# Kernel tuning notes

Hardware: AMD Instinct MI355X
Metric: run time of the kernel (lower is better)

Reference implementation:

```python
import jax, jax.numpy as jnp
import numpy as np

KERNEL = 9
EPS = 1e-5


def build_time_adj(t, kernel=KERNEL):
    # Faithful port of time_edge_index + utils.add_self_loops (all weights 1).
    # At[target, source] = 1 ; PyG edge list rows were [source=i, target=neighbor].
    p = (kernel - 1) // 2
    edges = []
    for i in range(t):
        if i < p:
            num_zeros_before = p - i
            elems = kernel - 1 - num_zeros_before
            before = i
            after = elems - before
            for j in range(before, 0, -1):
                edges.append((i, i - j))
            for j in range(after, 0, -1):
                edges.append((i, i + j))
        elif t - i <= p:
            num_zeros_after = p - (t - i) + 1
            elems = kernel - 1 - num_zeros_after
            before = kernel - 1 - p
            after = elems - before
            for j in range(before, 0, -1):
                edges.append((i, i - j))
            for j in range(after, 0, -1):
                edges.append((i, i + j))
        else:
            for j in range(1, p + 1):
                edges.append((i, i - j))
                edges.append((i, i + j))
    At = np.zeros((t, t), dtype=np.float32)
    for s, tg in edges:
        At[tg, s] = 1.0
    At[np.arange(t), np.arange(t)] = 1.0  # add_self_loops
    return At


def setup_inputs() -> dict:
    key = jax.random.key(0)
    ks = jax.random.split(key, 8)
    B, T, V, C = 64, 300, 25, 64
    x = jax.random.normal(ks[0], (B, T, V, C), dtype=jnp.float32)
    A = jax.random.uniform(ks[1], (3, V, V), dtype=jnp.float32)
    edge_importance = jnp.ones((3, V, V), dtype=jnp.float32)
    scale = 0.125  # ~xavier for 64x64
    W1 = jax.random.normal(ks[2], (C, C), dtype=jnp.float32) * scale
    W2 = jax.random.normal(ks[3], (C, C), dtype=jnp.float32) * scale
    W3 = jax.random.normal(ks[4], (C, C), dtype=jnp.float32) * scale
    Wt = jax.random.normal(ks[5], (C, C), dtype=jnp.float32) * scale
    b1 = jnp.zeros((C,), jnp.float32)
    b2 = jnp.zeros((C,), jnp.float32)
    b3 = jnp.zeros((C,), jnp.float32)
    bt = jnp.zeros((C,), jnp.float32)
    gamma = jnp.ones((C,), jnp.float32)
    beta = jnp.zeros((C,), jnp.float32)
    return {"x": x, "A": A, "edge_importance": edge_importance,
            "W1": W1, "b1": b1, "W2": W2, "b2": b2, "W3": W3, "b3": b3,
            "Wt": Wt, "bt": bt, "gamma": gamma, "beta": beta}


def reference(x, A, edge_importance, W1, b1, W2, b2, W3, b3, Wt, bt, gamma, beta):
    B, T, V, C = x.shape
    I = jnp.eye(V, dtype=x.dtype)
    Ae = A * edge_importance  # [3,V,V]

    # ---- Net_nodes: 3 spatial GCNConv branches summed (gcn_norm, self-loops) ----
    out = jnp.zeros((B, T, V, W1.shape[1]), dtype=x.dtype)
    for Ai, W, b in ((Ae[0], W1, b1), (Ae[1], W2, b2), (Ae[2], W3, b3)):
        Ad = Ai * (1.0 - I) + I                      # fill_diag(adj, 1.0)
        d = Ad.sum(axis=1)
        dinv = jnp.where(d > 0, d ** -0.5, 0.0)
        An = dinv[:, None] * Ad * dinv[None, :]      # D^-1/2 (A+I) D^-1/2
        out = out + jnp.einsum('vu,btuc->btvc', An, x @ W) + b

    def bn(h):  # BatchNorm2d over (B,T,V) per channel, training-mode stats
        m = h.mean(axis=(0, 1, 2))
        v = h.var(axis=(0, 1, 2))
        return (h - m) * jax.lax.rsqrt(v + EPS) * gamma + beta

    h = jax.nn.relu(bn(out))

    # ---- temporal GCNConv (normalize=False, unit edge weights, self loops) ----
    At = jnp.asarray(build_time_adj(T))              # [T,T] banded 0/1
    h = jnp.einsum('ts,bsvc->btvc', At, h @ Wt) + bt

    h = bn(h)  # same bn_2d module reused; dropout is identity in eval
    # residual=False, stride=1 -> x_res = 0, no sampling
    return jax.nn.relu(h)
```

## Files before the change

kernel.cpp:

```cpp
#include <hip/hip_runtime.h>

typedef unsigned short u16;
typedef unsigned int   u32;
typedef _Float16       f16;
typedef _Float16 f16x8 __attribute__((ext_vector_type(8)));
typedef float    f32x4 __attribute__((ext_vector_type(4)));

#define B_  64
#define T_  300
#define V_  25
#define C_  64
#define ROWS (B_*T_)
#define ROWE (V_*C_)
#define NSTAT 480000.0f
#define EPS_ 1e-5f
#define TTILE 30
#define K2BLK 1200
#define NWID  4800

__device__ __forceinline__ float b2f(u16 u) {
    union { u32 i; float f; } v; v.i = ((u32)u) << 16; return v.f;
}
__device__ __forceinline__ u16 f2b(float f) {
    union { float f; u32 i; } v; v.f = f;
    u32 x = v.i;
    u32 r = x + 0x7fffu + ((x >> 16) & 1u);
    return (u16)(r >> 16);
}
__device__ __forceinline__ u32 pk2h(float a, float b) {
    union { f16 h[2]; u32 u; } p;
    p.h[0] = (f16)a; p.h[1] = (f16)b;
    return p.u;
}
__device__ __forceinline__ u16 h2u(float v) {
    union { f16 h; u16 u; } p; p.h = (f16)v; return p.u;
}
__device__ __forceinline__ float u2h(u16 u) {
    union { u16 u; f16 h; } p; p.u = u; return (float)p.h;
}

template<bool F32>
__device__ __forceinline__ float ldv(const void* p, size_t i) {
    if (F32) return ((const float*)p)[i];
    return b2f(((const u16*)p)[i]);
}

template<bool F32> struct Geo { static const int STR = F32 ? 3200 : 1600; };

__global__ void k0_detect(const void* W1raw, int* flag)
{
    __shared__ float red[256];
    const u16* p = (const u16*)W1raw;
    float mx = 0.0f;
    for (int i = threadIdx.x; i < 4096; i += 256) {
        float v = fabsf(b2f(p[i]));
        if (v == v) mx = fmaxf(mx, v);
    }
    red[threadIdx.x] = mx;
    __syncthreads();
    for (int s = 128; s > 0; s >>= 1) {
        if (threadIdx.x < s) red[threadIdx.x] = fmaxf(red[threadIdx.x], red[threadIdx.x + s]);
        __syncthreads();
    }
    if (threadIdx.x == 0) flag[0] = (red[0] > 1e10f) ? 1 : 0;
}

template<bool F32>
__global__ void k1_prep(const int* __restrict__ flag,
                        const void* A, const void* E,
                        const void* W1, const void* W2, const void* W3,
                        const void* Wt,
                        const void* b1, const void* b2, const void* b3,
                        u16* __restrict__ anf, u16* __restrict__ wcatT,
                        u16* __restrict__ wtT, float* __restrict__ bsum)
{
    if (flag[0] != (F32 ? 1 : 0)) return;
    __shared__ float dinvL[75];
    const int tid = threadIdx.x;
    if (tid < 75) {
        int i = tid / 25, v = tid % 25;
        float d = 1.0f;
        for (int u = 0; u < 25; ++u)
            if (u != v) d += ldv<F32>(A, (i*25+v)*25+u) * ldv<F32>(E, (i*25+v)*25+u);
        dinvL[tid] = (d > 0.0f) ? rsqrtf(d) : 0.0f;
    }
    __syncthreads();
    for (int idx = tid; idx < 3072; idx += 256) {
        int fr = idx >> 9, lane = (idx >> 3) & 63, j = idx & 7;
        int i = fr >> 1, nt = fr & 1;
        int v = nt*16 + (lane & 15);
        int u = ((lane >> 4) << 3) + j;
        float val = 0.0f;
        if (v < 25 && u < 25) {
            float ad = (u == v) ? 1.0f
                     : ldv<F32>(A, (i*25+v)*25+u) * ldv<F32>(E, (i*25+v)*25+u);
            val = dinvL[i*25+v] * ad * dinvL[i*25+u];
        }
        anf[idx] = h2u(val);
    }
    for (int idx = tid; idx < 13824; idx += 256) {
        int i = idx / 4608;
        int rem = idx - i*4608;
        int c = rem / 72, k = rem - (rem/72)*72;
        float val = 0.0f;
        if (k < 64) {
            const void* W = (i == 0) ? W1 : ((i == 1) ? W2 : W3);
            val = ldv<F32>(W, k*64 + c);
        }
        wcatT[idx] = h2u(val);
    }
    for (int idx = tid; idx < 4608; idx += 256) {
        int c = idx / 72, k = idx - (idx/72)*72;
        float val = (k < 64) ? ldv<F32>(Wt, k*64 + c) : 0.0f;
        wtT[idx] = h2u(val);
    }
    if (tid < 64) bsum[tid] = ldv<F32>(b1, tid) + ldv<F32>(b2, tid) + ldv<F32>(b3, tid);
}

template<bool F32>
__global__ __launch_bounds__(256, 3) void k2_mfma(
    const int* __restrict__ flag, const void* x,
    const u16* __restrict__ wcatT, const u16* __restrict__ anf,
    u16* __restrict__ out1, u16* __restrict__ halo, float* __restrict__ p1)
{
    if (flag[0] != (F32 ? 1 : 0)) return;
    const int STR = Geo<F32>::STR;

    __shared__ f16 xfS[4][32*64];
    __shared__ u16 xwS[4][64*64];

    const int tid = threadIdx.x, lane = tid & 63, w = tid >> 6;
    const int lo = lane & 15, hi = lane >> 4;
    f16* xf = xfS[w];
    u16* xw = xwS[w];

    for (int q = lane; q < 224; q += 64) ((u32*)xf)[800 + q] = 0u;

    const int wid = blockIdx.x*4 + w;

    float ss[16], sq[16];
    #pragma unroll
    for (int i = 0; i < 16; ++i) { ss[i] = 0.0f; sq[i] = 0.0f; }

    #pragma unroll 1
    for (int rr = 0; rr < 4; ++rr) {
        const int row = wid*4 + rr;

        for (int q = lane; q < 200; q += 64) {
            const int u = q >> 3, g = q & 7;
            float v0,v1,v2,v3,v4,v5,v6,v7;
            if (F32) {
                float4 a4 = ((const float4*)x)[(size_t)row*400 + q*2];
                float4 b4 = ((const float4*)x)[(size_t)row*400 + q*2 + 1];
                v0=a4.x; v1=a4.y; v2=a4.z; v3=a4.w;
                v4=b4.x; v5=b4.y; v6=b4.z; v7=b4.w;
            } else {
                union { uint4 u4; u16 s[8]; } t4;
                t4.u4 = ((const uint4*)x)[(size_t)row*200 + q];
                v0=b2f(t4.s[0]); v1=b2f(t4.s[1]); v2=b2f(t4.s[2]); v3=b2f(t4.s[3]);
                v4=b2f(t4.s[4]); v5=b2f(t4.s[5]); v6=b2f(t4.s[6]); v7=b2f(t4.s[7]);
            }
            uint4 st = make_uint4(pk2h(v0,v1), pk2h(v2,v3), pk2h(v4,v5), pk2h(v6,v7));
            *(uint4*)&xf[u*64 + ((g ^ (u & 7)) << 3)] = st;
        }

        f32x4 acc[4][2];
        #pragma unroll
        for (int m = 0; m < 4; ++m) {
            acc[m][0] = f32x4{0.f,0.f,0.f,0.f};
            acc[m][1] = f32x4{0.f,0.f,0.f,0.f};
        }

        #pragma unroll 1
        for (int i = 0; i < 3; ++i) {
            f16x8 wfr[4][2];
            #pragma unroll
            for (int nt = 0; nt < 4; ++nt)
                #pragma unroll
                for (int ks = 0; ks < 2; ++ks)
                    wfr[nt][ks] = *(const f16x8*)&wcatT[
                        (size_t)(i*64 + nt*16 + lo)*72 + ks*32 + (hi << 3)];
            f16x8 an0 = *(const f16x8*)&anf[((i*2 + 0)*64 + lane)*8];
            f16x8 an1 = *(const f16x8*)&anf[((i*2 + 1)*64 + lane)*8];

            #pragma unroll
            for (int mt = 0; mt < 2; ++mt) {
                const int mrow = mt*16 + lo;
                f16x8 a0 = *(const f16x8*)&xf[mrow*64 + ((hi ^ (lo & 7)) << 3)];
                f16x8 a1 = *(const f16x8*)&xf[mrow*64 + (((4|hi) ^ (lo & 7)) << 3)];
                const int gu  = mt*2 + (hi >> 1);
                const int off = (hi & 1)*4;
                #pragma unroll
                for (int nt = 0; nt < 4; ++nt) {
                    f32x4 d = f32x4{0.f,0.f,0.f,0.f};
                    d = __builtin_amdgcn_mfma_f32_16x16x32_f16(a0, wfr[nt][0], d, 0, 0, 0);
                    d = __builtin_amdgcn_mfma_f32_16x16x32_f16(a1, wfr[nt][1], d, 0, 0, 0);
                    const int c = nt*16 + lo;
                    *(uint2*)&xw[c*64 + ((gu ^ (lo & 7)) << 3) + off] =
                        make_uint2(pk2h(d[0], d[1]), pk2h(d[2], d[3]));
                }
            }

            #pragma unroll
            for (int mt2 = 0; mt2 < 4; ++mt2) {
                f16x8 a = *(const f16x8*)&xw[(mt2*16 + lo)*64 + ((hi ^ (lo & 7)) << 3)];
                acc[mt2][0] = __builtin_amdgcn_mfma_f32_16x16x32_f16(a, an0, acc[mt2][0], 0, 0, 0);
                acc[mt2][1] = __builtin_amdgcn_mfma_f32_16x16x32_f16(a, an1, acc[mt2][1], 0, 0, 0);
            }
        }

        const int b = row / T_;
        const int t = row - b*T_;
        const int tm = t % TTILE;
        const bool hbd = (tm < 4) || (tm >= TTILE - 4);
        u16* hrow = nullptr;
        if (hbd) {
            const int slot = tm < 4 ? tm : tm - 22;
            hrow = halo + (((size_t)b*10 + t/TTILE)*8 + slot)*ROWE;
        }
        u16* orow = out1 + (size_t)row*STR;
        #pragma unroll
        for (int mt2 = 0; mt2 < 4; ++mt2) {
            const int c0 = mt2*16 + hi*4;
            #pragma unroll
            for (int nt2 = 0; nt2 < 2; ++nt2) {
                const int v = nt2*16 + lo;
                const float o0 = acc[mt2][nt2][0];
                const float o1 = acc[mt2][nt2][1];
                const float o2 = acc[mt2][nt2][2];
                const float o3 = acc[mt2][nt2][3];
                ss[mt2*4+0] += o0; sq[mt2*4+0] += o0*o0;
                ss[mt2*4+1] += o1; sq[mt2*4+1] += o1*o1;
                ss[mt2*4+2] += o2; sq[mt2*4+2] += o2*o2;
                ss[mt2*4+3] += o3; sq[mt2*4+3] += o3*o3;
                if (v < 25) {
                    ushort4 pk;
                    pk.x = f2b(o0); pk.y = f2b(o1); pk.z = f2b(o2); pk.w = f2b(o3);
                    *(ushort4*)&orow[v*64 + c0] = pk;
                    if (hbd) *(ushort4*)&hrow[v*64 + c0] = pk;
                }
            }
        }
    }

    #pragma unroll
    for (int si = 0; si < 16; ++si) {
        #pragma unroll
        for (int off = 1; off < 16; off <<= 1) {
            ss[si] += __shfl_xor(ss[si], off);
            sq[si] += __shfl_xor(sq[si], off);
        }
    }
    if (lo == 0) {
        #pragma unroll
        for (int si = 0; si < 16; ++si) {
            const int c = (si >> 2)*16 + hi*4 + (si & 3);
            p1[(size_t)wid*128 + c]      = ss[si];
            p1[(size_t)wid*128 + 64 + c] = sq[si];
        }
    }
}

__global__ __launch_bounds__(128) void k_reduce(const float* __restrict__ in,
                                                int n, float* __restrict__ outq)
{
    const int t = threadIdx.x;
    float s = 0.0f;
    for (int r = blockIdx.x; r < n; r += 64) s += in[(size_t)r*128 + t];
    outq[(size_t)blockIdx.x*128 + t] = s;
}

template<bool F32>
__global__ void k_bnstats(const int* __restrict__ flag,
                          const float* __restrict__ q,
                          const void* gamma, const void* beta,
                          const float* __restrict__ mb, int useb,
                          float* __restrict__ scale, float* __restrict__ shift)
{
    if (flag[0] != (F32 ? 1 : 0)) return;
    __shared__ float redL[512];
    const int tid = threadIdx.x, c = tid & 63, g = tid >> 6;
    float s = 0.0f, ssq = 0.0f;
    for (int r = g; r < 64; r += 4) { s += q[r*128 + c]; ssq += q[r*128 + 64 + c]; }
    redL[g*64 + c] = s; redL[256 + g*64 + c] = ssq;
    __syncthreads();
    if (tid < 64) {
        const float S  = redL[tid] + redL[64+tid] + redL[128+tid] + redL[192+tid];
        const float SS = redL[256+tid] + redL[320+tid] + redL[384+tid] + redL[448+tid];
        const float my  = S / NSTAT;
        const float var = SS / NSTAT - my*my;
        const float m   = my + (useb ? mb[tid] : 0.0f);
        const float rstd = rsqrtf(var + EPS_);
        const float sc = ldv<F32>(gamma, tid) * rstd;
        scale[tid] = sc;
        shift[tid] = ldv<F32>(beta, tid) - m * sc;
    }
}

template<bool F32>
__device__ __forceinline__ const u16* row_ptr(const u16* out1, const u16* halo,
                                              int b, int s, int t0)
{
    if (s >= t0 && s < t0 + TTILE)
        return &out1[((size_t)b*T_ + s) * Geo<F32>::STR];
    const int tile = s / TTILE, rem = s % TTILE;
    const int slot = rem < 4 ? rem : rem - 22;
    return &halo[(((size_t)b*10 + tile)*8 + slot) * ROWE];
}

template<bool F32>
__global__ __launch_bounds__(256, 3) void k3_temporal(
    const int* __restrict__ flag,
    u16* out1, const u16* __restrict__ halo,
    const u16* __restrict__ wtT, const void* bt,
    const float* __restrict__ sc1, const float* __restrict__ sh1,
    float* __restrict__ p2)
{
    if (flag[0] != (F32 ? 1 : 0)) return;
    const int STR = Geo<F32>::STR;

    __shared__ u16   ring[10*1600];
    __shared__ f16   hsumH[32*72];
    __shared__ u16   zL[1600];
    __shared__ float redL[256];

    const int tid = threadIdx.x, lane = tid & 63, w = tid >> 6;
    const int b = blockIdx.y, t0 = blockIdx.x * TTILE;
    const bool act = (tid < 200);

    for (int i = tid; i < 252; i += 256) ((u32*)&hsumH[25*72])[i] = 0u;

    float hacc[8];
    #pragma unroll
    for (int e = 0; e < 8; ++e) hacc[e] = 0.0f;
    const int c0u = (tid*8) & 63;
    const int vrow = tid >> 3;
    float S1[8], H1[8];
    #pragma unroll
    for (int e = 0; e < 8; ++e) { S1[e] = sc1[c0u+e]; H1[e] = sh1[c0u+e]; }

    const int ntp = w >> 1, mt = w & 1;
    f16x8 wfr[2][2];
    #pragma unroll
    for (int ntl = 0; ntl < 2; ++ntl)
        #pragma unroll
        for (int ks = 0; ks < 2; ++ks)
            wfr[ntl][ks] = *(const f16x8*)&wtT[
                ((ntp*2+ntl)*16 + (lane & 15))*72 + ks*32 + ((lane >> 4) << 3)];
    float btv[2];
    #pragma unroll
    for (int ntl = 0; ntl < 2; ++ntl)
        btv[ntl] = ldv<F32>(bt, (ntp*2+ntl)*16 + (lane & 15));

    {
        int slo = t0 - 4; if (slo < 0) slo = 0;
        for (int s = slo; s <= t0 + 4; ++s) {
            const u16* xr = row_ptr<F32>(out1, halo, b, s, t0);
            if (act) {
                uint4 xv = *(const uint4*)&xr[tid*8];
                const u16* xs = (const u16*)&xv;
                u16 hb[8];
                #pragma unroll
                for (int e = 0; e < 8; ++e) {
                    float hv = fmaf(b2f(xs[e]), S1[e], H1[e]);
                    hv = hv > 0.0f ? hv : 0.0f;
                    hb[e] = f2b(hv);
                    hacc[e] += b2f(hb[e]);
                }
                *(uint4*)&ring[(s%10)*1600 + tid*8] = *(uint4*)hb;
            }
        }
        if (act) {
            u16 hs[8];
            #pragma unroll
            for (int e = 0; e < 8; ++e) hs[e] = h2u(hacc[e]);
            *(uint4*)&hsumH[vrow*72 + c0u] = *(uint4*)hs;
        }
    }
    __syncthreads();

    float zs[2] = {0.f, 0.f}, zq[2] = {0.f, 0.f};

    for (int t = t0; t < t0 + TTILE; ++t) {
        {
            const int arow = (mt*16 + (lane & 15))*72 + ((lane >> 4) << 3);
            f16x8 a0 = *(const f16x8*)&hsumH[arow];
            f16x8 a1 = *(const f16x8*)&hsumH[arow + 32];
            #pragma unroll
            for (int ntl = 0; ntl < 2; ++ntl) {
                f32x4 d = f32x4{btv[ntl], btv[ntl], btv[ntl], btv[ntl]};
                d = __builtin_amdgcn_mfma_f32_16x16x32_f16(a0, wfr[ntl][0], d, 0, 0, 0);
                d = __builtin_amdgcn_mfma_f32_16x16x32_f16(a1, wfr[ntl][1], d, 0, 0, 0);
                const int cc = (ntp*2+ntl)*16 + (lane & 15);
                #pragma unroll
                for (int j = 0; j < 4; ++j) {
                    const int v = mt*16 + ((lane >> 4) << 2) + j;
                    if (v < 25) {
                        zs[ntl] += d[j]; zq[ntl] += d[j]*d[j];
                        zL[v*64 + cc] = h2u(d[j]);
                    }
                }
            }
        }
        __syncthreads();

        if (tid < 200)
            *(uint4*)&out1[((size_t)b*T_ + t)*STR + tid*8] = ((const uint4*)zL)[tid];

        if (t + 1 < t0 + TTILE) {
            const int snew = t + 5, sold = t - 4;
            if (act) {
                if (snew < T_) {
                    const u16* xr = row_ptr<F32>(out1, halo, b, snew, t0);
                    uint4 xv = *(const uint4*)&xr[tid*8];
                    const u16* xs = (const u16*)&xv;
                    u16 hb[8];
                    #pragma unroll
                    for (int e = 0; e < 8; ++e) {
                        float hv = fmaf(b2f(xs[e]), S1[e], H1[e]);
                        hv = hv > 0.0f ? hv : 0.0f;
                        hb[e] = f2b(hv);
                        hacc[e] += b2f(hb[e]);
                    }
                    *(uint4*)&ring[(snew%10)*1600 + tid*8] = *(uint4*)hb;
                }
                if (sold >= 0) {
                    uint4 ov = *(const uint4*)&ring[(sold%10)*1600 + tid*8];
                    const u16* os = (const u16*)&ov;
                    #pragma unroll
                    for (int e = 0; e < 8; ++e) hacc[e] -= b2f(os[e]);
                }
                u16 hs[8];
                #pragma unroll
                for (int e = 0; e < 8; ++e) hs[e] = h2u(hacc[e]);
                *(uint4*)&hsumH[vrow*72 + c0u] = *(uint4*)hs;
            }
        }
        __syncthreads();
    }

    #pragma unroll
    for (int ntl = 0; ntl < 2; ++ntl) {
        #pragma unroll
        for (int off = 16; off < 64; off <<= 1) {
            zs[ntl] += __shfl_xor(zs[ntl], off);
            zq[ntl] += __shfl_xor(zq[ntl], off);
        }
    }
    if (lane < 16) {
        redL[w*32 + lane]            = zs[0];
        redL[w*32 + 16 + lane]       = zs[1];
        redL[128 + w*32 + lane]      = zq[0];
        redL[128 + w*32 + 16 + lane] = zq[1];
    }
    __syncthreads();
    if (tid < 64) {
        const int c = tid;
        const int ntg = c >> 4, pr = ntg >> 1, ntl = ntg & 1, l = c & 15;
        const int w0 = pr*2, w1 = pr*2 + 1;
        float s = redL[w0*32 + ntl*16 + l] + redL[w1*32 + ntl*16 + l];
        float q = redL[128 + w0*32 + ntl*16 + l] + redL[128 + w1*32 + ntl*16 + l];
        const int blk = blockIdx.y * (T_/TTILE) + blockIdx.x;
        p2[(size_t)blk*128 + c]      = s;
        p2[(size_t)blk*128 + 64 + c] = q;
    }
}

template<bool F32>
__global__ __launch_bounds__(256) void k4_final(
    const int* __restrict__ flag,
    const float* __restrict__ sc2, const float* __restrict__ sh2,
    void* outp)
{
    if (flag[0] != (F32 ? 1 : 0)) return;
    const int tid = threadIdx.x;

    if (!F32) {
        const size_t NQ = (size_t)ROWS * 200;
        const size_t stride = (size_t)gridDim.x * blockDim.x;
        size_t q = (size_t)blockIdx.x * blockDim.x + tid;
        const int c0 = ((int)(q & 7)) * 8;
        float S2[8], H2[8];
        #pragma unroll
        for (int e = 0; e < 8; ++e) { S2[e] = sc2[c0+e]; H2[e] = sh2[c0+e]; }
        u16* z = (u16*)outp;
        for (; q < NQ; q += stride) {
            union { uint4 u4; u16 s[8]; } zv;
            zv.u4 = *(const uint4*)&z[q*8];
            u16 ob[8];
            #pragma unroll
            for (int e = 0; e < 8; ++e) {
                float oo = fmaf(u2h(zv.s[e]), S2[e], H2[e]);
                ob[e] = f2b(oo > 0.0f ? oo : 0.0f);
            }
            *(uint4*)&z[q*8] = *(uint4*)ob;
        }
    } else {
        const int STR = Geo<true>::STR;
        const int c0u = (tid*8) & 63;
        float S2[8], H2[8];
        #pragma unroll
        for (int e = 0; e < 8; ++e) { S2[e] = sc2[c0u+e]; H2[e] = sh2[c0u+e]; }
        const int r0 = blockIdx.x * 10;
        u16* z = (u16*)outp;
        for (int r = 0; r < 10; ++r) {
            const int row = r0 + r;
            uint4 zv;
            if (tid < 200) zv = *(const uint4*)&z[(size_t)row*STR + tid*8];
            __syncthreads();
            if (tid < 200) {
                const u16* zp = (const u16*)&zv;
                float o[8];
                #pragma unroll
                for (int e = 0; e < 8; ++e) {
                    float oo = fmaf(u2h(zp[e]), S2[e], H2[e]);
                    o[e] = oo > 0.0f ? oo : 0.0f;
                }
                float* dst = (float*)outp + (size_t)row*ROWE + tid*8;
                *(float4*)dst     = float4{o[0], o[1], o[2], o[3]};
                *(float4*)(dst+4) = float4{o[4], o[5], o[6], o[7]};
            }
            __syncthreads();
        }
    }
}

extern "C" void kernel_launch(void* const* d_in, const int* in_sizes, int n_in,
                              void* d_out, int out_size, void* d_ws, size_t ws_size,
                              hipStream_t stream)
{
    const void* x     = d_in[0];
    const void* A     = d_in[1];
    const void* E     = d_in[2];
    const void* W1    = d_in[3];
    const void* b1    = d_in[4];
    const void* W2    = d_in[5];
    const void* b2    = d_in[6];
    const void* W3    = d_in[7];
    const void* b3    = d_in[8];
    const void* Wt    = d_in[9];
    const void* bt    = d_in[10];
    const void* gamma = d_in[11];
    const void* beta  = d_in[12];

    u16* out1 = (u16*)d_out;

    int*   flag = (int*)d_ws;
    float* wsf  = (float*)d_ws;
    float* bsum = wsf + 4;
    float* sc1  = bsum + 64;
    float* sh1  = sc1 + 64;
    float* sc2  = sh1 + 64;
    float* sh2  = sc2 + 64;
    float* p1   = sh2 + 64;
    float* p2   = p1 + (size_t)NWID*128;
    float* q1   = p2 + 640*128;
    float* q2   = q1 + 64*128;
    u16*  halo  = (u16*)(q2 + 64*128);
    u16*  wcatT = halo + (size_t)5120*1600;
    u16*  anf   = wcatT + 13824;
    u16*  wtT   = anf + 3072;

    const long NX = (long)B_*T_*V_*C_;
    int mode = -1;
    if (n_in > 0) {
        if      (in_sizes[0] == (int)(NX*2)) mode = 0;
        else if (in_sizes[0] == (int)(NX*4)) mode = 1;
    }
    const bool do_b = (mode != 1), do_f = (mode != 0);

    hipLaunchKernelGGL(k0_detect, dim3(1), dim3(256), 0, stream, W1, flag);

    if (do_b) hipLaunchKernelGGL(k1_prep<false>, dim3(1), dim3(256), 0, stream,
                       flag, A, E, W1, W2, W3, Wt, b1, b2, b3, anf, wcatT, wtT, bsum);
    if (do_f) hipLaunchKernelGGL(k1_prep<true>, dim3(1), dim3(256), 0, stream,
                       flag, A, E, W1, W2, W3, Wt, b1, b2, b3, anf, wcatT, wtT, bsum);

    if (do_b) hipLaunchKernelGGL(k2_mfma<false>, dim3(K2BLK), dim3(256), 0, stream,
                       flag, x, wcatT, anf, out1, halo, p1);
    if (do_f) hipLaunchKernelGGL(k2_mfma<true>, dim3(K2BLK), dim3(256), 0, stream,
                       flag, x, wcatT, anf, out1, halo, p1);

    hipLaunchKernelGGL(k_reduce, dim3(64), dim3(128), 0, stream, p1, NWID, q1);

    if (do_b) hipLaunchKernelGGL(k_bnstats<false>, dim3(1), dim3(256), 0, stream,
                       flag, q1, gamma, beta, bsum, 1, sc1, sh1);
    if (do_f) hipLaunchKernelGGL(k_bnstats<true>, dim3(1), dim3(256), 0, stream,
                       flag, q1, gamma, beta, bsum, 1, sc1, sh1);

    if (do_b) hipLaunchKernelGGL(k3_temporal<false>, dim3(10, 64), dim3(256), 0, stream,
                       flag, out1, halo, wtT, bt, sc1, sh1, p2);
    if (do_f) hipLaunchKernelGGL(k3_temporal<true>, dim3(10, 64), dim3(256), 0, stream,
                       flag, out1, halo, wtT, bt, sc1, sh1, p2);

    hipLaunchKernelGGL(k_reduce, dim3(64), dim3(128), 0, stream, p2, 640, q2);

    if (do_b) hipLaunchKernelGGL(k_bnstats<false>, dim3(1), dim3(256), 0, stream,
                       flag, q2, gamma, beta, bsum, 0, sc2, sh2);
    if (do_f) hipLaunchKernelGGL(k_bnstats<true>, dim3(1), dim3(256), 0, stream,
                       flag, q2, gamma, beta, bsum, 0, sc2, sh2);

    if (do_b) hipLaunchKernelGGL(k4_final<false>, dim3(2048), dim3(256), 0, stream,
                       flag, sc2, sh2, d_out);
    if (do_f) hipLaunchKernelGGL(k4_final<true>, dim3(1920), dim3(256), 0, stream,
                       flag, sc2, sh2, d_out);
}
```

Before: 439.8 us.

## Restructure spatial GCN kernel to share rows across waves and hoist weight fragments

The spatial MFMA kernel now packs 4 (b,t) rows into a 112-row M dimension and loads x straight from global memory into MFMA fragments, skipping the LDS staging. Each wave computes 48 of the 192 concatenated output channels for all four rows, so weight and adjacency fragments load once into registers and stay there. Results go to a shared padded LDS buffer, and after a block barrier each wave runs the adjacency matmul for one row. BN partial sums are reduced per block in LDS before they are written. This removes redundant per-wave weight reloads and separate x staging, at the cost of block-wide barriers and wasted MFMA rows from padding 100 to 112.

```diff
diff --git a/kernel.cpp b/kernel.cpp
--- a/kernel.cpp
+++ b/kernel.cpp
@@ -15,8 +15,8 @@
 #define NSTAT 480000.0f
 #define EPS_ 1e-5f
 #define TTILE 30
-#define K2BLK 1200
-#define NWID  4800
+#define K2BLK 2400
+#define YSP 104
 
 __device__ __forceinline__ float b2f(u16 u) {
     union { u32 i; float f; } v; v.i = ((u32)u) << 16; return v.f;
@@ -71,7 +71,7 @@
                         const void* W1, const void* W2, const void* W3,
                         const void* Wt,
                         const void* b1, const void* b2, const void* b3,
-                        u16* __restrict__ anf, u16* __restrict__ wcatT,
+                        u16* __restrict__ anf2, u16* __restrict__ wcatT,
                         u16* __restrict__ wtT, float* __restrict__ bsum)
 {
     if (flag[0] != (F32 ? 1 : 0)) return;
@@ -87,16 +87,17 @@
     __syncthreads();
     for (int idx = tid; idx < 3072; idx += 256) {
         int fr = idx >> 9, lane = (idx >> 3) & 63, j = idx & 7;
-        int i = fr >> 1, nt = fr & 1;
-        int v = nt*16 + (lane & 15);
-        int u = ((lane >> 4) << 3) + j;
+        int ks = fr >> 1, nt = fr & 1;
+        int v  = nt*16 + (lane & 15);
+        int up = ks*32 + ((lane >> 4) << 3) + j;
+        int i  = up >> 5, u = up & 31;
         float val = 0.0f;
         if (v < 25 && u < 25) {
             float ad = (u == v) ? 1.0f
                      : ldv<F32>(A, (i*25+v)*25+u) * ldv<F32>(E, (i*25+v)*25+u);
             val = dinvL[i*25+v] * ad * dinvL[i*25+u];
         }
-        anf[idx] = h2u(val);
+        anf2[idx] = h2u(val);
     }
     for (int idx = tid; idx < 13824; idx += 256) {
         int i = idx / 4608;
@@ -120,127 +121,139 @@
 template<bool F32>
 __global__ __launch_bounds__(256, 3) void k2_mfma(
     const int* __restrict__ flag, const void* x,
-    const u16* __restrict__ wcatT, const u16* __restrict__ anf,
+    const u16* __restrict__ wcatT, const u16* __restrict__ anf2,
     u16* __restrict__ out1, u16* __restrict__ halo, float* __restrict__ p1)
 {
     if (flag[0] != (F32 ? 1 : 0)) return;
     const int STR = Geo<F32>::STR;
 
-    __shared__ f16 xfS[4][32*64];
-    __shared__ u16 xwS[4][64*64];
+    __shared__ f16 ys[4][64*YSP];
 
     const int tid = threadIdx.x, lane = tid & 63, w = tid >> 6;
     const int lo = lane & 15, hi = lane >> 4;
-    f16* xf = xfS[w];
-    u16* xw = xwS[w];
-
-    for (int q = lane; q < 224; q += 64) ((u32*)xf)[800 + q] = 0u;
-
-    const int wid = blockIdx.x*4 + w;
+
+    f16x8 wfr[3][2];
+    #pragma unroll
+    for (int q = 0; q < 3; ++q)
+        #pragma unroll
+        for (int kc = 0; kc < 2; ++kc)
+            wfr[q][kc] = *(const f16x8*)&wcatT[
+                (size_t)((3*w + q)*16 + lo)*72 + kc*32 + (hi << 3)];
+    f16x8 anfr[3][2];
+    #pragma unroll
+    for (int ks = 0; ks < 3; ++ks)
+        #pragma unroll
+        for (int nt = 0; nt < 2; ++nt)
+            anfr[ks][nt] = *(const f16x8*)&anf2[((ks*2 + nt)*64 + lane)*8];
 
     float ss[16], sq[16];
     #pragma unroll
     for (int i = 0; i < 16; ++i) { ss[i] = 0.0f; sq[i] = 0.0f; }
 
     #pragma unroll 1
-    for (int rr = 0; rr < 4; ++rr) {
-        const int row = wid*4 + rr;
-
-        for (int q = lane; q < 200; q += 64) {
-            const int u = q >> 3, g = q & 7;
-            float v0,v1,v2,v3,v4,v5,v6,v7;
+    for (int bb = 0; bb < 2; ++bb) {
+        const int r0 = blockIdx.x*8 + bb*4;
+
+        #pragma unroll
+        for (int mt = 0; mt < 7; ++mt) {
+            const int m  = mt*16 + lo;
+            const int rA = (m*293) >> 13;
+            const int uA = m - 28*rA;
+            const int ua = (uA < 25) ? uA : 0;
+            const size_t xb = (size_t)(r0 + rA)*1600 + (size_t)ua*64 + (hi << 3);
+            f16x8 a0, a1;
             if (F32) {
-                float4 a4 = ((const float4*)x)[(size_t)row*400 + q*2];
-                float4 b4 = ((const float4*)x)[(size_t)row*400 + q*2 + 1];
-                v0=a4.x; v1=a4.y; v2=a4.z; v3=a4.w;
-                v4=b4.x; v5=b4.y; v6=b4.z; v7=b4.w;
+                const float* xp = (const float*)x + xb;
+                float4 fa = *(const float4*)xp, fb = *(const float4*)(xp + 4);
+                a0[0]=(f16)fa.x; a0[1]=(f16)fa.y; a0[2]=(f16)fa.z; a0[3]=(f16)fa.w;
+                a0[4]=(f16)fb.x; a0[5]=(f16)fb.y; a0[6]=(f16)fb.z; a0[7]=(f16)fb.w;
+                const float* xq = xp + 32;
+                float4 ga = *(const float4*)xq, gb = *(const float4*)(xq + 4);
+                a1[0]=(f16)ga.x; a1[1]=(f16)ga.y; a1[2]=(f16)ga.z; a1[3]=(f16)ga.w;
+                a1[4]=(f16)gb.x; a1[5]=(f16)gb.y; a1[6]=(f16)gb.z; a1[7]=(f16)gb.w;
             } else {
-                union { uint4 u4; u16 s[8]; } t4;
-                t4.u4 = ((const uint4*)x)[(size_t)row*200 + q];
-                v0=b2f(t4.s[0]); v1=b2f(t4.s[1]); v2=b2f(t4.s[2]); v3=b2f(t4.s[3]);
-                v4=b2f(t4.s[4]); v5=b2f(t4.s[5]); v6=b2f(t4.s[6]); v7=b2f(t4.s[7]);
-            }
-            uint4 st = make_uint4(pk2h(v0,v1), pk2h(v2,v3), pk2h(v4,v5), pk2h(v6,v7));
-            *(uint4*)&xf[u*64 + ((g ^ (u & 7)) << 3)] = st;
-        }
+                union { uint4 q4; u16 s[8]; } ta, tb;
+                ta.q4 = *(const uint4*)((const u16*)x + xb);
+                tb.q4 = *(const uint4*)((const u16*)x + xb + 32);
+                #pragma unroll
+                for (int e = 0; e < 8; ++e) {
+                    a0[e] = (f16)b2f(ta.s[e]);
+                    a1[e] = (f16)b2f(tb.s[e]);
+                }
+            }
+            const int md = mt*16 + (hi << 2);
+            const int rD = (md*293) >> 13;
+            const int u0 = md - 28*rD;
+            #pragma unroll
+            for (int q = 0; q < 3; ++q) {
+                f32x4 d = f32x4{0.f, 0.f, 0.f, 0.f};
+                d = __builtin_amdgcn_mfma_f32_16x16x32_f16(a0, wfr[q][0], d, 0, 0, 0);
+                d = __builtin_amdgcn_mfma_f32_16x16x32_f16(a1, wfr[q][1], d, 0, 0, 0);
+                const int np = (3*w + q)*16 + lo;
+                const int ib = np >> 6, cb = np & 63;
+                f16* yr = &ys[rD][cb*YSP + ib*32 + u0];
+                if (u0 <= 20) {
+                    *(uint2*)yr = make_uint2(pk2h(d[0], d[1]), pk2h(d[2], d[3]));
+                } else {
+                    *(uint4*)yr = make_uint4(pk2h(d[0], 0.0f), 0u, 0u, 0u);
+                }
+            }
+        }
+        __syncthreads();
 
         f32x4 acc[4][2];
         #pragma unroll
-        for (int m = 0; m < 4; ++m) {
-            acc[m][0] = f32x4{0.f,0.f,0.f,0.f};
-            acc[m][1] = f32x4{0.f,0.f,0.f,0.f};
-        }
-
-        #pragma unroll 1
-        for (int i = 0; i < 3; ++i) {
-            f16x8 wfr[4][2];
+        for (int mt = 0; mt < 4; ++mt) {
+            acc[mt][0] = f32x4{0.f,0.f,0.f,0.f};
+            acc[mt][1] = f32x4{0.f,0.f,0.f,0.f};
+        }
+        #pragma unroll
+        for (int ks = 0; ks < 3; ++ks) {
             #pragma unroll
-            for (int nt = 0; nt < 4; ++nt)
+            for (int mt = 0; mt < 4; ++mt) {
+                f16x8 a = *(const f16x8*)&ys[w][
+                    (mt*16 + lo)*YSP + ks*32 + (hi << 3)];
+                acc[mt][0] = __builtin_amdgcn_mfma_f32_16x16x32_f16(a, anfr[ks][0], acc[mt][0], 0, 0, 0);
+                acc[mt][1] = __builtin_amdgcn_mfma_f32_16x16x32_f16(a, anfr[ks][1], acc[mt][1], 0, 0, 0);
+            }
+        }
+
+        {
+            const int row = r0 + w;
+            const int b = row / T_;
+            const int t = row - b*T_;
+            const int tm = t % TTILE;
+            const bool hbd = (tm < 4) || (tm >= TTILE - 4);
+            u16* hrow = nullptr;
+            if (hbd) {
+                const int slot = tm < 4 ? tm : tm - 22;
+                hrow = halo + (((size_t)b*10 + t/TTILE)*8 + slot)*ROWE;
+            }
+            u16* orow = out1 + (size_t)row*STR;
+            #pragma unroll
+            for (int mt = 0; mt < 4; ++mt) {
+                const int c0 = mt*16 + (hi << 2);
                 #pragma unroll
-                for (int ks = 0; ks < 2; ++ks)
-                    wfr[nt][ks] = *(const f16x8*)&wcatT[
-                        (size_t)(i*64 + nt*16 + lo)*72 + ks*32 + (hi << 3)];
-            f16x8 an0 = *(const f16x8*)&anf[((i*2 + 0)*64 + lane)*8];
-            f16x8 an1 = *(const f16x8*)&anf[((i*2 + 1)*64 + lane)*8];
-
-            #pragma unroll
-            for (int mt = 0; mt < 2; ++mt) {
-                const int mrow = mt*16 + lo;
-                f16x8 a0 = *(const f16x8*)&xf[mrow*64 + ((hi ^ (lo & 7)) << 3)];
-                f16x8 a1 = *(const f16x8*)&xf[mrow*64 + (((4|hi) ^ (lo & 7)) << 3)];
-                const int gu  = mt*2 + (hi >> 1);
-                const int off = (hi & 1)*4;
-                #pragma unroll
-                for (int nt = 0; nt < 4; ++nt) {
-                    f32x4 d = f32x4{0.f,0.f,0.f,0.f};
-                    d = __builtin_amdgcn_mfma_f32_16x16x32_f16(a0, wfr[nt][0], d, 0, 0, 0);
-                    d = __builtin_amdgcn_mfma_f32_16x16x32_f16(a1, wfr[nt][1], d, 0, 0, 0);
-                    const int c = nt*16 + lo;
-                    *(uint2*)&xw[c*64 + ((gu ^ (lo & 7)) << 3) + off] =
-                        make_uint2(pk2h(d[0], d[1]), pk2h(d[2], d[3]));
-                }
-            }
-
-            #pragma unroll
-            for (int mt2 = 0; mt2 < 4; ++mt2) {
-                f16x8 a = *(const f16x8*)&xw[(mt2*16 + lo)*64 + ((hi ^ (lo & 7)) << 3)];
-                acc[mt2][0] = __builtin_amdgcn_mfma_f32_16x16x32_f16(a, an0, acc[mt2][0], 0, 0, 0);
-                acc[mt2][1] = __builtin_amdgcn_mfma_f32_16x16x32_f16(a, an1, acc[mt2][1], 0, 0, 0);
-            }
-        }
-
-        const int b = row / T_;
-        const int t = row - b*T_;
-        const int tm = t % TTILE;
-        const bool hbd = (tm < 4) || (tm >= TTILE - 4);
-        u16* hrow = nullptr;
-        if (hbd) {
-            const int slot = tm < 4 ? tm : tm - 22;
-            hrow = halo + (((size_t)b*10 + t/TTILE)*8 + slot)*ROWE;
-        }
-        u16* orow = out1 + (size_t)row*STR;
-        #pragma unroll
-        for (int mt2 = 0; mt2 < 4; ++mt2) {
-            const int c0 = mt2*16 + hi*4;
-            #pragma unroll
-            for (int nt2 = 0; nt2 < 2; ++nt2) {
-                const int v = nt2*16 + lo;
-                const float o0 = acc[mt2][nt2][0];
-                const float o1 = acc[mt2][nt2][1];
-                const float o2 = acc[mt2][nt2][2];
-                const float o3 = acc[mt2][nt2][3];
-                ss[mt2*4+0] += o0; sq[mt2*4+0] += o0*o0;
-                ss[mt2*4+1] += o1; sq[mt2*4+1] += o1*o1;
-                ss[mt2*4+2] += o2; sq[mt2*4+2] += o2*o2;
-                ss[mt2*4+3] += o3; sq[mt2*4+3] += o3*o3;
-                if (v < 25) {
-                    ushort4 pk;
-                    pk.x = f2b(o0); pk.y = f2b(o1); pk.z = f2b(o2); pk.w = f2b(o3);
-                    *(ushort4*)&orow[v*64 + c0] = pk;
-                    if (hbd) *(ushort4*)&hrow[v*64 + c0] = pk;
-                }
-            }
-        }
+                for (int nt = 0; nt < 2; ++nt) {
+                    const int v = nt*16 + lo;
+                    if (v < 25) {
+                        const float o0 = acc[mt][nt][0];
+                        const float o1 = acc[mt][nt][1];
+                        const float o2 = acc[mt][nt][2];
+                        const float o3 = acc[mt][nt][3];
+                        ss[mt*4+0] += o0; sq[mt*4+0] += o0*o0;
+                        ss[mt*4+1] += o1; sq[mt*4+1] += o1*o1;
+                        ss[mt*4+2] += o2; sq[mt*4+2] += o2*o2;
+                        ss[mt*4+3] += o3; sq[mt*4+3] += o3*o3;
+                        ushort4 pk;
+                        pk.x = f2b(o0); pk.y = f2b(o1); pk.z = f2b(o2); pk.w = f2b(o3);
+                        *(ushort4*)&orow[v*64 + c0] = pk;
+                        if (hbd) *(ushort4*)&hrow[v*64 + c0] = pk;
+                    }
+                }
+            }
+        }
+        __syncthreads();
     }
 
     #pragma unroll
@@ -251,13 +264,21 @@
             sq[si] += __shfl_xor(sq[si], off);
         }
     }
+    float* red = (float*)ys;
     if (lo == 0) {
         #pragma unroll
         for (int si = 0; si < 16; ++si) {
-            const int c = (si >> 2)*16 + hi*4 + (si & 3);
-            p1[(size_t)wid*128 + c]      = ss[si];
-            p1[(size_t)wid*128 + 64 + c] = sq[si];
-        }
+            const int c = ((si >> 2) << 4) + (hi << 2) + (si & 3);
+            red[w*64 + c]        = ss[si];
+            red[256 + w*64 + c]  = sq[si];
+        }
+    }
+    __syncthreads();
+    if (tid < 128) {
+        const int isq = tid >> 6, c = tid & 63;
+        const float* rb = red + isq*256;
+        p1[(size_t)blockIdx.x*128 + isq*64 + c] =
+            rb[c] + rb[64 + c] + rb[128 + c] + rb[192 + c];
     }
 }
 
@@ -553,13 +574,13 @@
     float* sc2  = sh1 + 64;
     float* sh2  = sc2 + 64;
     float* p1   = sh2 + 64;
-    float* p2   = p1 + (size_t)NWID*128;
+    float* p2   = p1 + (size_t)K2BLK*128;
     float* q1   = p2 + 640*128;
     float* q2   = q1 + 64*128;
     u16*  halo  = (u16*)(q2 + 64*128);
     u16*  wcatT = halo + (size_t)5120*1600;
-    u16*  anf   = wcatT + 13824;
-    u16*  wtT   = anf + 3072;
+    u16*  anf2  = wcatT + 13824;
+    u16*  wtT   = anf2 + 3072;
 
     const long NX = (long)B_*T_*V_*C_;
     int mode = -1;
@@ -572,16 +593,16 @@
     hipLaunchKernelGGL(k0_detect, dim3(1), dim3(256), 0, stream, W1, flag);
 
     if (do_b) hipLaunchKernelGGL(k1_prep<false>, dim3(1), dim3(256), 0, stream,
-                       flag, A, E, W1, W2, W3, Wt, b1, b2, b3, anf, wcatT, wtT, bsum);
+                       flag, A, E, W1, W2, W3, Wt, b1, b2, b3, anf2, wcatT, wtT, bsum);
     if (do_f) hipLaunchKernelGGL(k1_prep<true>, dim3(1), dim3(256), 0, stream,
-                       flag, A, E, W1, W2, W3, Wt, b1, b2, b3, anf, wcatT, wtT, bsum);
+                       flag, A, E, W1, W2, W3, Wt, b1, b2, b3, anf2, wcatT, wtT, bsum);
 
     if (do_b) hipLaunchKernelGGL(k2_mfma<false>, dim3(K2BLK), dim3(256), 0, stream,
-                       flag, x, wcatT, anf, out1, halo, p1);
+                       flag, x, wcatT, anf2, out1, halo, p1);
     if (do_f) hipLaunchKernelGGL(k2_mfma<true>, dim3(K2BLK), dim3(256), 0, stream,
-                       flag, x, wcatT, anf, out1, halo, p1);
-
-    hipLaunchKernelGGL(k_reduce, dim3(64), dim3(128), 0, stream, p1, NWID, q1);
+                       flag, x, wcatT, anf2, out1, halo, p1);
+
+    hipLaunchKernelGGL(k_reduce, dim3(64), dim3(128), 0, stream, p1, K2BLK, q1);
 
     if (do_b) hipLaunchKernelGGL(k_bnstats<false>, dim3(1), dim3(256), 0, stream,
                        flag, q1, gamma, beta, bsum, 1, sc1, sh1);
```

Result: faster. 428.3 us (-2.6%).

## Batch four rows per block in spatial GEMM and warp-specialize temporal kernel

Applied to the files above, without the earlier changes.

The spatial kernel now makes a whole 256-thread block work on four rows together. The rows are packed into one padded shared tile of 112 M-rows so the X·W MFMA covers 7 tiles instead of per-wave padded 32-row tiles, the A-hat fragments are hoisted, and more blocks are launched. The temporal kernel grows to 512 threads: four waves do MFMA compute while four others stream the sliding-window sums and write back the previous step's output, using double-buffered hsum and z tiles. This is meant to cut wasted MFMA padding and to overlap memory work with compute, at the cost of extra block barriers and more LDS and threads per block.

```diff
diff --git a/kernel.cpp b/kernel.cpp
--- a/kernel.cpp
+++ b/kernel.cpp
@@ -15,8 +15,9 @@
 #define NSTAT 480000.0f
 #define EPS_ 1e-5f
 #define TTILE 30
-#define K2BLK 1200
-#define NWID  4800
+#define K2BLK 4800
+#define XFS 74
+#define XWS 42
 
 __device__ __forceinline__ float b2f(u16 u) {
     union { u32 i; float f; } v; v.i = ((u32)u) << 16; return v.f;
@@ -118,7 +119,7 @@
 }
 
 template<bool F32>
-__global__ __launch_bounds__(256, 3) void k2_mfma(
+__global__ __launch_bounds__(256, 4) void k2_mfma(
     const int* __restrict__ flag, const void* x,
     const u16* __restrict__ wcatT, const u16* __restrict__ anf,
     u16* __restrict__ out1, u16* __restrict__ halo, float* __restrict__ p1)
@@ -126,89 +127,98 @@
     if (flag[0] != (F32 ? 1 : 0)) return;
     const int STR = Geo<F32>::STR;
 
-    __shared__ f16 xfS[4][32*64];
-    __shared__ u16 xwS[4][64*64];
-
-    const int tid = threadIdx.x, lane = tid & 63, w = tid >> 6;
+    __shared__ f16 xf[112*XFS];
+    __shared__ u16 xw[256*XWS];
+
+    const int tid  = threadIdx.x;
+    const int lane = tid & 63, w = tid >> 6;
     const int lo = lane & 15, hi = lane >> 4;
-    f16* xf = xfS[w];
-    u16* xw = xwS[w];
-
-    for (int q = lane; q < 224; q += 64) ((u32*)xf)[800 + q] = 0u;
-
-    const int wid = blockIdx.x*4 + w;
-
-    float ss[16], sq[16];
+    const int r0   = blockIdx.x * 4;
+
+    for (int q4 = tid; q4 < 1600; q4 += 256) {
+        int r = (q4 * 10486) >> 22;
+        int rem = q4 - 400*r;
+        float v0, v1, v2, v3;
+        if (F32) {
+            float4 t4 = ((const float4*)x)[(size_t)(r0+r)*400 + rem];
+            v0 = t4.x; v1 = t4.y; v2 = t4.z; v3 = t4.w;
+        } else {
+            ushort4 t4 = ((const ushort4*)x)[(size_t)(r0+r)*400 + rem];
+            v0 = b2f(t4.x); v1 = b2f(t4.y); v2 = b2f(t4.z); v3 = b2f(t4.w);
+        }
+        int u = rem >> 4, k0 = (rem & 15) << 2;
+        int m = r*28 + u;
+        *(uint2*)&xf[m*XFS + k0] = make_uint2(pk2h(v0, v1), pk2h(v2, v3));
+    }
+    for (int idx = tid; idx < 444; idx += 256) {
+        int j   = idx / 37;
+        int off = idx - 37*j;
+        int rr = j / 3, p = j - 3*rr;
+        ((u32*)xf)[(rr*28 + 25 + p)*(XFS/2) + off] = 0u;
+    }
+    *(uint2*)&xw[tid*XWS + 28] = make_uint2(0u, 0u);
+
+    f16x8 anfr[3][2];
     #pragma unroll
-    for (int i = 0; i < 16; ++i) { ss[i] = 0.0f; sq[i] = 0.0f; }
-
-    #pragma unroll 1
-    for (int rr = 0; rr < 4; ++rr) {
-        const int row = wid*4 + rr;
-
-        for (int q = lane; q < 200; q += 64) {
-            const int u = q >> 3, g = q & 7;
-            float v0,v1,v2,v3,v4,v5,v6,v7;
-            if (F32) {
-                float4 a4 = ((const float4*)x)[(size_t)row*400 + q*2];
-                float4 b4 = ((const float4*)x)[(size_t)row*400 + q*2 + 1];
-                v0=a4.x; v1=a4.y; v2=a4.z; v3=a4.w;
-                v4=b4.x; v5=b4.y; v6=b4.z; v7=b4.w;
-            } else {
-                union { uint4 u4; u16 s[8]; } t4;
-                t4.u4 = ((const uint4*)x)[(size_t)row*200 + q];
-                v0=b2f(t4.s[0]); v1=b2f(t4.s[1]); v2=b2f(t4.s[2]); v3=b2f(t4.s[3]);
-                v4=b2f(t4.s[4]); v5=b2f(t4.s[5]); v6=b2f(t4.s[6]); v7=b2f(t4.s[7]);
+    for (int i = 0; i < 3; ++i)
+        #pragma unroll
+        for (int nt = 0; nt < 2; ++nt)
+            anfr[i][nt] = *(const f16x8*)&anf[((i*2 + nt)*64 + lane)*8];
+
+    const int c0 = w*16 + (hi << 2);
+
+    f32x4 acc[4][2];
+    #pragma unroll
+    for (int j = 0; j < 4; ++j) {
+        acc[j][0] = f32x4{0.f, 0.f, 0.f, 0.f};
+        acc[j][1] = f32x4{0.f, 0.f, 0.f, 0.f};
+    }
+
+    __syncthreads();
+
+    #pragma unroll
+    for (int i = 0; i < 3; ++i) {
+        f16x8 wfr[4][2];
+        #pragma unroll
+        for (int nt = 0; nt < 4; ++nt)
+            #pragma unroll
+            for (int ks = 0; ks < 2; ++ks)
+                wfr[nt][ks] = *(const f16x8*)&wcatT[
+                    (size_t)(i*64 + nt*16 + lo)*72 + ks*32 + (hi << 3)];
+
+        for (int mt = w; mt < 7; mt += 4) {
+            const int arow = (mt*16 + lo)*XFS + (hi << 3);
+            f16x8 a0 = *(const f16x8*)&xf[arow];
+            f16x8 a1 = *(const f16x8*)&xf[arow + 32];
+            const int m0 = mt*16 + (hi << 2);
+            const int r  = (m0 * 293) >> 13;
+            const int u0 = m0 - 28*r;
+            #pragma unroll
+            for (int nt = 0; nt < 4; ++nt) {
+                f32x4 d = f32x4{0.f, 0.f, 0.f, 0.f};
+                d = __builtin_amdgcn_mfma_f32_16x16x32_f16(a0, wfr[nt][0], d, 0, 0, 0);
+                d = __builtin_amdgcn_mfma_f32_16x16x32_f16(a1, wfr[nt][1], d, 0, 0, 0);
+                const int cc = nt*16 + lo;
+                *(uint2*)&xw[(r*64 + cc)*XWS + u0] =
+                    make_uint2(pk2h(d[0], d[1]), pk2h(d[2], d[3]));
             }
-            uint4 st = make_uint4(pk2h(v0,v1), pk2h(v2,v3), pk2h(v4,v5), pk2h(v6,v7));
-            *(uint4*)&xf[u*64 + ((g ^ (u & 7)) << 3)] = st;
-        }
-
-        f32x4 acc[4][2];
-        #pragma unroll
-        for (int m = 0; m < 4; ++m) {
-            acc[m][0] = f32x4{0.f,0.f,0.f,0.f};
-            acc[m][1] = f32x4{0.f,0.f,0.f,0.f};
-        }
-
-        #pragma unroll 1
-        for (int i = 0; i < 3; ++i) {
-            f16x8 wfr[4][2];
-            #pragma unroll
-            for (int nt = 0; nt < 4; ++nt)
-                #pragma unroll
-                for (int ks = 0; ks < 2; ++ks)
-                    wfr[nt][ks] = *(const f16x8*)&wcatT[
-                        (size_t)(i*64 + nt*16 + lo)*72 + ks*32 + (hi << 3)];
-            f16x8 an0 = *(const f16x8*)&anf[((i*2 + 0)*64 + lane)*8];
-            f16x8 an1 = *(const f16x8*)&anf[((i*2 + 1)*64 + lane)*8];
-
-            #pragma unroll
-            for (int mt = 0; mt < 2; ++mt) {
-                const int mrow = mt*16 + lo;
-                f16x8 a0 = *(const f16x8*)&xf[mrow*64 + ((hi ^ (lo & 7)) << 3)];
-                f16x8 a1 = *(const f16x8*)&xf[mrow*64 + (((4|hi) ^ (lo & 7)) << 3)];
-                const int gu  = mt*2 + (hi >> 1);
-                const int off = (hi & 1)*4;
-                #pragma unroll
-                for (int nt = 0; nt < 4; ++nt) {
-                    f32x4 d = f32x4{0.f,0.f,0.f,0.f};
-                    d = __builtin_amdgcn_mfma_f32_16x16x32_f16(a0, wfr[nt][0], d, 0, 0, 0);
-                    d = __builtin_amdgcn_mfma_f32_16x16x32_f16(a1, wfr[nt][1], d, 0, 0, 0);
-                    const int c = nt*16 + lo;
-                    *(uint2*)&xw[c*64 + ((gu ^ (lo & 7)) << 3) + off] =
-                        make_uint2(pk2h(d[0], d[1]), pk2h(d[2], d[3]));
-                }
-            }
-
-            #pragma unroll
-            for (int mt2 = 0; mt2 < 4; ++mt2) {
-                f16x8 a = *(const f16x8*)&xw[(mt2*16 + lo)*64 + ((hi ^ (lo & 7)) << 3)];
-                acc[mt2][0] = __builtin_amdgcn_mfma_f32_16x16x32_f16(a, an0, acc[mt2][0], 0, 0, 0);
-                acc[mt2][1] = __builtin_amdgcn_mfma_f32_16x16x32_f16(a, an1, acc[mt2][1], 0, 0, 0);
-            }
-        }
-
+        }
+        __syncthreads();
+
+        #pragma unroll
+        for (int j = 0; j < 4; ++j) {
+            const int mt2 = w + 4*j;
+            f16x8 a = *(const f16x8*)&xw[(mt2*16 + lo)*XWS + (hi << 3)];
+            acc[j][0] = __builtin_amdgcn_mfma_f32_16x16x32_f16(a, anfr[i][0], acc[j][0], 0, 0, 0);
+            acc[j][1] = __builtin_amdgcn_mfma_f32_16x16x32_f16(a, anfr[i][1], acc[j][1], 0, 0, 0);
+        }
+        __syncthreads();
+    }
+
+    float ssum[4] = {0.f, 0.f, 0.f, 0.f}, ssq[4] = {0.f, 0.f, 0.f, 0.f};
+    #pragma unroll
+    for (int j = 0; j < 4; ++j) {
+        const int row = r0 + j;
         const int b = row / T_;
         const int t = row - b*T_;
         const int tm = t % TTILE;
@@ -220,43 +230,37 @@
         }
         u16* orow = out1 + (size_t)row*STR;
         #pragma unroll
-        for (int mt2 = 0; mt2 < 4; ++mt2) {
-            const int c0 = mt2*16 + hi*4;
-            #pragma unroll
-            for (int nt2 = 0; nt2 < 2; ++nt2) {
-                const int v = nt2*16 + lo;
-                const float o0 = acc[mt2][nt2][0];
-                const float o1 = acc[mt2][nt2][1];
-                const float o2 = acc[mt2][nt2][2];
-                const float o3 = acc[mt2][nt2][3];
-                ss[mt2*4+0] += o0; sq[mt2*4+0] += o0*o0;
-                ss[mt2*4+1] += o1; sq[mt2*4+1] += o1*o1;
-                ss[mt2*4+2] += o2; sq[mt2*4+2] += o2*o2;
-                ss[mt2*4+3] += o3; sq[mt2*4+3] += o3*o3;
-                if (v < 25) {
-                    ushort4 pk;
-                    pk.x = f2b(o0); pk.y = f2b(o1); pk.z = f2b(o2); pk.w = f2b(o3);
-                    *(ushort4*)&orow[v*64 + c0] = pk;
-                    if (hbd) *(ushort4*)&hrow[v*64 + c0] = pk;
-                }
+        for (int nt = 0; nt < 2; ++nt) {
+            const int v = nt*16 + lo;
+            if (v < 25) {
+                float o0 = acc[j][nt][0];
+                float o1 = acc[j][nt][1];
+                float o2 = acc[j][nt][2];
+                float o3 = acc[j][nt][3];
+                ssum[0] += o0; ssq[0] += o0*o0;
+                ssum[1] += o1; ssq[1] += o1*o1;
+                ssum[2] += o2; ssq[2] += o2*o2;
+                ssum[3] += o3; ssq[3] += o3*o3;
+                ushort4 pk;
+                pk.x = f2b(o0); pk.y = f2b(o1); pk.z = f2b(o2); pk.w = f2b(o3);
+                *(ushort4*)&orow[v*64 + c0] = pk;
+                if (hbd) *(ushort4*)&hrow[v*64 + c0] = pk;
             }
         }
     }
-
     #pragma unroll
-    for (int si = 0; si < 16; ++si) {
+    for (int t = 0; t < 4; ++t) {
         #pragma unroll
         for (int off = 1; off < 16; off <<= 1) {
-            ss[si] += __shfl_xor(ss[si], off);
-            sq[si] += __shfl_xor(sq[si], off);
+            ssum[t] += __shfl_xor(ssum[t], off);
+            ssq[t]  += __shfl_xor(ssq[t],  off);
         }
     }
     if (lo == 0) {
         #pragma unroll
-        for (int si = 0; si < 16; ++si) {
-            const int c = (si >> 2)*16 + hi*4 + (si & 3);
-            p1[(size_t)wid*128 + c]      = ss[si];
-            p1[(size_t)wid*128 + 64 + c] = sq[si];
+        for (int t = 0; t < 4; ++t) {
+            p1[(size_t)blockIdx.x*128 + c0 + t]      = ssum[t];
+            p1[(size_t)blockIdx.x*128 + 64 + c0 + t] = ssq[t];
         }
     }
 }
@@ -309,7 +313,7 @@
 }
 
 template<bool F32>
-__global__ __launch_bounds__(256, 3) void k3_temporal(
+__global__ __launch_bounds__(512, 4) void k3_temporal(
     const int* __restrict__ flag,
     u16* out1, const u16* __restrict__ halo,
     const u16* __restrict__ wtT, const void* bt,
@@ -320,70 +324,74 @@
     const int STR = Geo<F32>::STR;
 
     __shared__ u16   ring[10*1600];
-    __shared__ f16   hsumH[32*72];
-    __shared__ u16   zL[1600];
+    __shared__ f16   hsumH[2*2304];
+    __shared__ u16   zL[2][1600];
     __shared__ float redL[256];
 
     const int tid = threadIdx.x, lane = tid & 63, w = tid >> 6;
     const int b = blockIdx.y, t0 = blockIdx.x * TTILE;
-    const bool act = (tid < 200);
-
-    for (int i = tid; i < 252; i += 256) ((u32*)&hsumH[25*72])[i] = 0u;
-
-    float hacc[8];
-    #pragma unroll
-    for (int e = 0; e < 8; ++e) hacc[e] = 0.0f;
-    const int c0u = (tid*8) & 63;
-    const int vrow = tid >> 3;
-    float S1[8], H1[8];
-    #pragma unroll
-    for (int e = 0; e < 8; ++e) { S1[e] = sc1[c0u+e]; H1[e] = sh1[c0u+e]; }
+    const bool isC = (w < 4);
+    const int tidW = tid - 256;
+    const bool actW = (!isC) && (tidW < 200);
+
+    for (int i = tid; i < 1152; i += 512) ((u32*)hsumH)[i] = 0u;
+
+    float hacc[8], S1[8], H1[8];
+    int c0u = 0, vrow = 0;
+    if (!isC) {
+        const int tt = (tidW < 200) ? tidW : 0;
+        c0u = (tt*8) & 63;
+        vrow = tt >> 3;
+        #pragma unroll
+        for (int e = 0; e < 8; ++e) {
+            hacc[e] = 0.0f; S1[e] = sc1[c0u+e]; H1[e] = sh1[c0u+e];
+        }
+    }
 
     const int ntp = w >> 1, mt = w & 1;
     f16x8 wfr[2][2];
-    #pragma unroll
-    for (int ntl = 0; ntl < 2; ++ntl)
-        #pragma unroll
-        for (int ks = 0; ks < 2; ++ks)
-            wfr[ntl][ks] = *(const f16x8*)&wtT[
-                ((ntp*2+ntl)*16 + (lane & 15))*72 + ks*32 + ((lane >> 4) << 3)];
-    float btv[2];
-    #pragma unroll
-    for (int ntl = 0; ntl < 2; ++ntl)
-        btv[ntl] = ldv<F32>(bt, (ntp*2+ntl)*16 + (lane & 15));
-
-    {
+    float btv[2] = {0.f, 0.f};
+    if (isC) {
+        #pragma unroll
+        for (int ntl = 0; ntl < 2; ++ntl) {
+            #pragma unroll
+            for (int ks = 0; ks < 2; ++ks)
+                wfr[ntl][ks] = *(const f16x8*)&wtT[
+                    ((ntp*2+ntl)*16 + (lane & 15))*72 + ks*32 + ((lane >> 4) << 3)];
+            btv[ntl] = ldv<F32>(bt, (ntp*2+ntl)*16 + (lane & 15));
+        }
+    }
+    __syncthreads();
+
+    if (actW) {
         int slo = t0 - 4; if (slo < 0) slo = 0;
         for (int s = slo; s <= t0 + 4; ++s) {
             const u16* xr = row_ptr<F32>(out1, halo, b, s, t0);
-            if (act) {
-                uint4 xv = *(const uint4*)&xr[tid*8];
-                const u16* xs = (const u16*)&xv;
-                u16 hb[8];
-                #pragma unroll
-                for (int e = 0; e < 8; ++e) {
-                    float hv = fmaf(b2f(xs[e]), S1[e], H1[e]);
-                    hv = hv > 0.0f ? hv : 0.0f;
-                    hb[e] = f2b(hv);
-                    hacc[e] += b2f(hb[e]);
-                }
-                *(uint4*)&ring[(s%10)*1600 + tid*8] = *(uint4*)hb;
+            uint4 xv = *(const uint4*)&xr[tidW*8];
+            const u16* xs = (const u16*)&xv;
+            u16 hb[8];
+            #pragma unroll
+            for (int e = 0; e < 8; ++e) {
+                float hv = fmaf(b2f(xs[e]), S1[e], H1[e]);
+                hv = hv > 0.0f ? hv : 0.0f;
+                hb[e] = f2b(hv);
+                hacc[e] += b2f(hb[e]);
             }
-        }
-        if (act) {
-            u16 hs[8];
-            #pragma unroll
-            for (int e = 0; e < 8; ++e) hs[e] = h2u(hacc[e]);
-            *(uint4*)&hsumH[vrow*72 + c0u] = *(uint4*)hs;
-        }
+            *(uint4*)&ring[(s%10)*1600 + tidW*8] = *(uint4*)hb;
+        }
+        u16 hs[8];
+        #pragma unroll
+        for (int e = 0; e < 8; ++e) hs[e] = h2u(hacc[e]);
+        *(uint4*)&hsumH[vrow*72 + c0u] = *(uint4*)hs;
     }
     __syncthreads();
 
     float zs[2] = {0.f, 0.f}, zq[2] = {0.f, 0.f};
 
     for (int t = t0; t < t0 + TTILE; ++t) {
-        {
-            const int arow = (mt*16 + (lane & 15))*72 + ((lane >> 4) << 3);
+        const int cur = (t - t0) & 1;
+        if (isC) {
+            const int arow = cur*2304 + (mt*16 + (lane & 15))*72 + ((lane >> 4) << 3);
             f16x8 a0 = *(const f16x8*)&hsumH[arow];
             f16x8 a1 = *(const f16x8*)&hsumH[arow + 32];
             #pragma unroll
@@ -397,22 +405,19 @@
                     const int v = mt*16 + ((lane >> 4) << 2) + j;
                     if (v < 25) {
                         zs[ntl] += d[j]; zq[ntl] += d[j]*d[j];
-                        zL[v*64 + cc] = h2u(d[j]);
+                        zL[cur][v*64 + cc] = h2u(d[j]);
                     }
                 }
             }
-        }
-        __syncthreads();
-
-        if (tid < 200)
-            *(uint4*)&out1[((size_t)b*T_ + t)*STR + tid*8] = ((const uint4*)zL)[tid];
-
-        if (t + 1 < t0 + TTILE) {
-            const int snew = t + 5, sold = t - 4;
-            if (act) {
+        } else {
+            if (t > t0 && actW)
+                *(uint4*)&out1[((size_t)b*T_ + (t-1))*STR + tidW*8] =
+                    *(const uint4*)&zL[cur^1][tidW*8];
+            if (t + 1 < t0 + TTILE && actW) {
+                const int snew = t + 5, sold = t - 4;
                 if (snew < T_) {
                     const u16* xr = row_ptr<F32>(out1, halo, b, snew, t0);
-                    uint4 xv = *(const uint4*)&xr[tid*8];
+                    uint4 xv = *(const uint4*)&xr[tidW*8];
                     const u16* xs = (const u16*)&xv;
                     u16 hb[8];
                     #pragma unroll
@@ -422,10 +427,10 @@
                         hb[e] = f2b(hv);
                         hacc[e] += b2f(hb[e]);
                     }
-                    *(uint4*)&ring[(snew%10)*1600 + tid*8] = *(uint4*)hb;
+                    *(uint4*)&ring[(snew%10)*1600 + tidW*8] = *(uint4*)hb;
                 }
                 if (sold >= 0) {
-                    uint4 ov = *(const uint4*)&ring[(sold%10)*1600 + tid*8];
+                    uint4 ov = *(const uint4*)&ring[(sold%10)*1600 + tidW*8];
                     const u16* os = (const u16*)&ov;
                     #pragma unroll
                     for (int e = 0; e < 8; ++e) hacc[e] -= b2f(os[e]);
@@ -433,11 +438,15 @@
                 u16 hs[8];
                 #pragma unroll
                 for (int e = 0; e < 8; ++e) hs[e] = h2u(hacc[e]);
-                *(uint4*)&hsumH[vrow*72 + c0u] = *(uint4*)hs;
+                *(uint4*)&hsumH[(cur^1)*2304 + vrow*72 + c0u] = *(uint4*)hs;
             }
         }
         __syncthreads();
     }
+
+    if (actW)
+        *(uint4*)&out1[((size_t)b*T_ + (t0 + TTILE - 1))*STR + tidW*8] =
+            *(const uint4*)&zL[(TTILE-1)&1][tidW*8];
 
     #pragma unroll
     for (int ntl = 0; ntl < 2; ++ntl) {
@@ -447,7 +456,7 @@
             zq[ntl] += __shfl_xor(zq[ntl], off);
         }
     }
-    if (lane < 16) {
+    if (isC && lane < 16) {
         redL[w*32 + lane]            = zs[0];
         redL[w*32 + 16 + lane]       = zs[1];
         redL[128 + w*32 + lane]      = zq[0];
@@ -553,7 +562,7 @@
     float* sc2  = sh1 + 64;
     float* sh2  = sc2 + 64;
     float* p1   = sh2 + 64;
-    float* p2   = p1 + (size_t)NWID*128;
+    float* p2   = p1 + (size_t)K2BLK*128;
     float* q1   = p2 + 640*128;
     float* q2   = q1 + 64*128;
     u16*  halo  = (u16*)(q2 + 64*128);
@@ -581,16 +590,16 @@
     if (do_f) hipLaunchKernelGGL(k2_mfma<true>, dim3(K2BLK), dim3(256), 0, stream,
                        flag, x, wcatT, anf, out1, halo, p1);
 
-    hipLaunchKernelGGL(k_reduce, dim3(64), dim3(128), 0, stream, p1, NWID, q1);
+    hipLaunchKernelGGL(k_reduce, dim3(64), dim3(128), 0, stream, p1, K2BLK, q1);
 
     if (do_b) hipLaunchKernelGGL(k_bnstats<false>, dim3(1), dim3(256), 0, stream,
                        flag, q1, gamma, beta, bsum, 1, sc1, sh1);
     if (do_f) hipLaunchKernelGGL(k_bnstats<true>, dim3(1), dim3(256), 0, stream,
                        flag, q1, gamma, beta, bsum, 1, sc1, sh1);
 
-    if (do_b) hipLaunchKernelGGL(k3_temporal<false>, dim3(10, 64), dim3(256), 0, stream,
+    if (do_b) hipLaunchKernelGGL(k3_temporal<false>, dim3(10, 64), dim3(512), 0, stream,
                        flag, out1, halo, wtT, bt, sc1, sh1, p2);
-    if (do_f) hipLaunchKernelGGL(k3_temporal<true>, dim3(10, 64), dim3(256), 0, stream,
+    if (do_f) hipLaunchKernelGGL(k3_temporal<true>, dim3(10, 64), dim3(512), 0, stream,
                        flag, out1, halo, wtT, bt, sc1, sh1, p2);
 
     hipLaunchKernelGGL(k_reduce, dim3(64), dim3(128), 0, stream, p2, 640, q2);
```

Measured after the change: 439.3 us. No clear change (-0.1%).
